# Kernel tuning notes

Measured on AMD Instinct MI355X. Metric: run time of the kernel, lower is better.

The kernel has to match this reference:

```python
import jax, jax.numpy as jnp
import numpy as np

LATENT_DIM = 512
NUM_EMBEDDINGS = 4096
COMMITMENT_COST = 0.25
N_TOKENS = 32768


def setup_inputs() -> dict:
    key = jax.random.key(0)
    k_z, k_e = jax.random.split(key)
    z = jax.random.normal(k_z, (N_TOKENS, LATENT_DIM), dtype=jnp.float32)
    # embedding.weight ~ U(-1/K, 1/K), matching the torch init
    emb = jax.random.uniform(
        k_e, (NUM_EMBEDDINGS, LATENT_DIM), dtype=jnp.float32,
        minval=-1.0 / NUM_EMBEDDINGS, maxval=1.0 / NUM_EMBEDDINGS)
    return {"z": z, "emb": emb}


def reference(z, emb):
    flat_z = z.reshape(-1, LATENT_DIM)  # [N, D]
    # squared L2 distances: ||z||^2 + ||e||^2 - 2 z.e^T  -> [N, K]
    distances = (
        jnp.sum(flat_z ** 2, axis=1, keepdims=True)
        + jnp.sum(emb ** 2, axis=1)
        - 2.0 * jnp.matmul(flat_z, emb.T)
    )
    encoding_indices = jnp.argmin(distances, axis=1)  # [N]
    quantized = emb[encoding_indices].reshape(z.shape)  # [N, D]

    q_latent_loss = jnp.mean((jax.lax.stop_gradient(quantized) - z) ** 2)
    commitment_loss = jnp.mean((quantized - jax.lax.stop_gradient(z)) ** 2)
    vq_loss = q_latent_loss + COMMITMENT_COST * commitment_loss

    # codebook usage perplexity (histogram instead of dense one-hot)
    n = flat_z.shape[0]
    counts = jnp.zeros((NUM_EMBEDDINGS,), jnp.float32).at[encoding_indices].add(1.0)
    avg_probs = counts / n
    perplexity = jnp.exp(-jnp.sum(avg_probs * jnp.log(avg_probs + 1e-10)))

    # straight-through estimator
    quantized_st = z + jax.lax.stop_gradient(quantized - z)
    return quantized_st, vq_loss, perplexity
```

## Files before the change

### kernel.cpp

```cpp
#include <hip/hip_runtime.h>

#define NTOK   32768
#define DIM    512
#define NCODE  4096
#define NELEM  (NTOK*DIM)
#define COMMIT 0.25
#define ESCALE 8192.0f
#define EINV   (1.0f/4096.0f)
#define KSCL   262144.0f
#define KOFF   65536.0f

#define OFF_Z8      0ULL
#define OFF_E8      16777216ULL
#define OFF_EN32    18874368ULL
#define OFF_ROWMIN  18890752ULL
#define OFF_COUNTS  19021824ULL
#define OFF_SSE     19038208ULL

typedef int   v8i  __attribute__((ext_vector_type(8)));
typedef float v16f __attribute__((ext_vector_type(16)));

#define GLOBAL_AS __attribute__((address_space(1)))
#define LDS_AS    __attribute__((address_space(3)))

__device__ __forceinline__ void gld16(const void* g, void* l) {
    __builtin_amdgcn_global_load_lds((const GLOBAL_AS unsigned int*)g,
                                     (LDS_AS unsigned int*)l, 16, 0, 0);
}

__global__ void conv_kernel(const float* __restrict__ z, const float* __restrict__ e,
                            unsigned* __restrict__ z8, unsigned* __restrict__ e8,
                            unsigned* __restrict__ counts, double* __restrict__ sse,
                            float* __restrict__ en32) {
    const int ZI = NELEM / 16;
    const int TI = ZI + (NCODE * DIM) / 16;
    int i = blockIdx.x * blockDim.x + threadIdx.x;
    if (i < NCODE) counts[i] = 0u;
    if (i < 256)   sse[i] = 0.0;
    if (i >= TI) return;
    const bool isEmb = (i >= ZI);
    const float4* src; unsigned* dst; int j; float sc;
    if (!isEmb) { src = (const float4*)z; dst = z8; j = i; sc = 1.0f; }
    else        { src = (const float4*)e; dst = e8; j = i - ZI; sc = ESCALE; }
    uint4 o;
    double nrm = 0.0;
#pragma unroll
    for (int q = 0; q < 4; q++) {
        float4 v = src[j * 4 + q];
        if (isEmb)
            nrm += (double)v.x*v.x + (double)v.y*v.y + (double)v.z*v.z + (double)v.w*v.w;
        int r = 0;
        r = __builtin_amdgcn_cvt_pk_fp8_f32(v.x * sc, v.y * sc, r, false);
        r = __builtin_amdgcn_cvt_pk_fp8_f32(v.z * sc, v.w * sc, r, true);
        (&o.x)[q] = (unsigned)r;
    }
    ((uint4*)dst)[j] = o;
    if (isEmb) {
#pragma unroll
        for (int off = 16; off; off >>= 1) nrm += __shfl_xor(nrm, off);
        if ((j & 31) == 0) en32[j >> 5] = (float)nrm;
    }
}

__global__ __launch_bounds__(256, 2)
void score_pass(const unsigned char* __restrict__ z8, const unsigned char* __restrict__ e8,
                const float* __restrict__ en32,
                const float* __restrict__ zf32, const float* __restrict__ embf,
                float* __restrict__ out, double* __restrict__ sse,
                unsigned* __restrict__ counts) {
    __shared__ __align__(16) unsigned char sB0[64 * 512];
    __shared__ __align__(16) unsigned char sB1[64 * 512];
    __shared__ __align__(16) float sEn[NCODE];
    const int tid = threadIdx.x;
    const int row0 = blockIdx.x * 64;
    const int wv = tid >> 6, ln = tid & 63;
    const int wm = wv & 1;
    const int wn = wv >> 1;
    const int c = ln & 31, h = ln >> 5;

#pragma unroll
    for (int s = 0; s < 8; s++) {
        int q = wv * 8 + s;
        int r = 2 * q + h;
        unsigned g = (unsigned)((ln & 31) ^ (r & 31));
        gld16(z8 + (size_t)(row0 + r) * 512 + g * 16u, sB1 + q * 1024);
    }
#pragma unroll
    for (int s = 0; s < 4; s++) {
        int chunk = wv * 4 + s;
        gld16((const unsigned char*)en32 + chunk * 1024 + (unsigned)(ln * 16),
              (unsigned char*)sEn + chunk * 1024);
    }

    unsigned eoff[8];
#pragma unroll
    for (int s = 0; s < 8; s++) {
        int q = wv * 8 + s;
        int r = 2 * q + h;
        unsigned g = (unsigned)((ln & 31) ^ (r & 31));
        eoff[s] = (unsigned)(r * 512) + g * 16u;
    }

    __builtin_amdgcn_sched_barrier(0);

#pragma unroll
    for (int s = 0; s < 8; s++)
        gld16(e8 + eoff[s], sB0 + (wv * 8 + s) * 1024);

    asm volatile("s_waitcnt vmcnt(8)" ::: "memory");
    __builtin_amdgcn_s_barrier();

    const int mrow = (wm * 32 + c) * 512;
    const int nrow = (wn * 32 + c) * 512;
    v8i za[8];
#pragma unroll
    for (int kt = 0; kt < 8; kt++) {
        int G = kt * 4 + 2 * h;
        uint4 x0 = *(const uint4*)(sB1 + mrow + (((G    ) ^ c) * 16));
        uint4 x1 = *(const uint4*)(sB1 + mrow + (((G + 1) ^ c) * 16));
        za[kt] = (v8i){(int)x0.x, (int)x0.y, (int)x0.z, (int)x0.w,
                       (int)x1.x, (int)x1.y, (int)x1.z, (int)x1.w};
    }
    asm volatile("s_waitcnt lgkmcnt(0)" ::: "memory");
    __builtin_amdgcn_s_barrier();

#pragma unroll
    for (int s = 0; s < 8; s++)
        gld16(e8 + 32768 + eoff[s], sB1 + (wv * 8 + s) * 1024);

    unsigned runmin[16];
#pragma unroll
    for (int reg = 0; reg < 16; reg++) runmin[reg] = 0xFFFFFFFFu;

    for (int ct = 0; ct < 64; ct++) {
        if (ct == 63) asm volatile("s_waitcnt vmcnt(0)" ::: "memory");
        else          asm volatile("s_waitcnt vmcnt(8)" ::: "memory");
        __builtin_amdgcn_s_barrier();

        const unsigned char* sB = (ct & 1) ? sB1 : sB0;
        float en = sEn[ct * 64 + wn * 32 + c];
        v16f acc0 = (v16f)(0.0f), acc1 = (v16f)(0.0f);
#pragma unroll
        for (int kt = 0; kt < 8; kt++) {
            int G = kt * 4 + 2 * h;
            uint4 y0 = *(const uint4*)(sB + nrow + (((G    ) ^ c) * 16));
            uint4 y1 = *(const uint4*)(sB + nrow + (((G + 1) ^ c) * 16));
            v8i b = (v8i){(int)y0.x, (int)y0.y, (int)y0.z, (int)y0.w,
                          (int)y1.x, (int)y1.y, (int)y1.z, (int)y1.w};
            if (kt & 1)
                acc1 = __builtin_amdgcn_mfma_scale_f32_32x32x64_f8f6f4(
                    za[kt], b, acc1, 0, 0, 0, 0x7F, 0, 0x7F);
            else
                acc0 = __builtin_amdgcn_mfma_scale_f32_32x32x64_f8f6f4(
                    za[kt], b, acc0, 0, 0, 0, 0x7F, 0, 0x7F);
        }

        unsigned n = (unsigned)(ct * 64 + wn * 32 + c);
#pragma unroll
        for (int reg = 0; reg < 16; reg++) {
            float s = en - (acc0[reg] + acc1[reg]) * EINV;
            unsigned kq = (unsigned)fmaf(s, KSCL, KOFF);
            unsigned p = (kq << 12) | n;
            runmin[reg] = runmin[reg] < p ? runmin[reg] : p;
        }

        asm volatile("s_waitcnt lgkmcnt(0)" ::: "memory");
        __builtin_amdgcn_s_barrier();

        if (ct < 62) {
            unsigned char* sD = (ct & 1) ? sB1 : sB0;
            const unsigned char* ebase = e8 + (size_t)(ct + 2) * 32768;
#pragma unroll
            for (int s = 0; s < 8; s++)
                gld16(ebase + eoff[s], sD + (wv * 8 + s) * 1024);
        }
    }

    __syncthreads();
    unsigned* tmp = (unsigned*)sB0;
#pragma unroll
    for (int reg = 0; reg < 16; reg++) {
        unsigned v = runmin[reg];
#pragma unroll
        for (int off = 1; off < 32; off <<= 1) {
            unsigned o = (unsigned)__shfl_xor((int)v, off);
            v = v < o ? v : o;
        }
        if (c == 0) {
            int rr = (reg & 3) + 8 * (reg >> 2) + 4 * h;
            tmp[(wm * 2 + wn) * 32 + rr] = v;
        }
    }
    __syncthreads();
    unsigned* rmin = (unsigned*)sB1;
    if (tid < 64) {
        int wmb = tid >> 5, rr = tid & 31;
        unsigned v0 = tmp[(wmb * 2 + 0) * 32 + rr];
        unsigned v1 = tmp[(wmb * 2 + 1) * 32 + rr];
        unsigned best = v0 < v1 ? v0 : v1;
        rmin[tid] = best & 0xFFFu;
        atomicAdd(&counts[best & 0xFFFu], 1u);
    }
    __syncthreads();

    const float4* zf = (const float4*)(zf32 + (size_t)row0 * 512);
    float4*       of = (float4*)(out + (size_t)row0 * 512);
    const float4* ef = (const float4*)embf;
    double loc = 0.0;
#pragma unroll 4
    for (int it = 0; it < 32; it++) {
        int idx = tid + it * 256;
        int row = idx >> 7, col = idx & 127;
        unsigned code = rmin[row];
        float4 zv = zf[idx];
        float4 q  = ef[code * 128 + col];
        float dx = q.x - zv.x, dy = q.y - zv.y, dz = q.z - zv.z, dw = q.w - zv.w;
        of[idx] = make_float4(zv.x + dx, zv.y + dy, zv.z + dz, zv.w + dw);
        loc += (double)dx*dx + (double)dy*dy + (double)dz*dz + (double)dw*dw;
    }
    for (int off = 32; off; off >>= 1) loc += __shfl_down(loc, off);
    double* sw = (double*)sEn;
    if (ln == 0) sw[wv] = loc;
    __syncthreads();
    if (tid == 0)
        atomicAdd(&sse[blockIdx.x & 255], sw[0] + sw[1] + sw[2] + sw[3]);
}

__global__ void finalize(const unsigned* __restrict__ counts, const double* __restrict__ sse,
                         float* __restrict__ out) {
    __shared__ double sh[256], sv[256];
    double h = 0.0;
    for (int b = threadIdx.x; b < NCODE; b += 256) {
        double p = (double)counts[b] / (double)NTOK;
        h += p * log(p + 1e-10);
    }
    sh[threadIdx.x] = h;
    sv[threadIdx.x] = sse[threadIdx.x];
    __syncthreads();
    for (int off = 128; off > 0; off >>= 1) {
        if (threadIdx.x < off) {
            sh[threadIdx.x] += sh[threadIdx.x + off];
            sv[threadIdx.x] += sv[threadIdx.x + off];
        }
        __syncthreads();
    }
    if (threadIdx.x == 0) {
        out[NELEM]     = (float)((1.0 + COMMIT) * sv[0] / (double)NELEM);
        out[NELEM + 1] = (float)exp(-sh[0]);
    }
}

extern "C" void kernel_launch(void* const* d_in, const int* in_sizes, int n_in,
                              void* d_out, int out_size, void* d_ws, size_t ws_size,
                              hipStream_t stream) {
    const float* z   = (const float*)d_in[0];
    const float* emb = (const float*)d_in[1];
    float* out = (float*)d_out;
    char* ws = (char*)d_ws;

    unsigned* z8 = (unsigned*)(ws + OFF_Z8);
    unsigned* e8 = (unsigned*)(ws + OFF_E8);
    float*    en32 = (float*)(ws + OFF_EN32);
    unsigned* counts = (unsigned*)(ws + OFF_COUNTS);
    double*   sse    = (double*)(ws + OFF_SSE);

    conv_kernel<<<(NELEM/16 + (NCODE*DIM)/16 + 255) / 256, 256, 0, stream>>>(
        z, emb, z8, e8, counts, sse, en32);

    score_pass<<<NTOK / 64, 256, 0, stream>>>((const unsigned char*)z8,
                                              (const unsigned char*)e8, en32,
                                              z, emb, out, sse, counts);

    finalize<<<1, 256, 0, stream>>>(counts, sse, out);
}
```

Measured before the change: 217.1 us.

## Fuse z FP8 conversion into score kernel, drop z8 workspace round-trip

The z-to-FP8 conversion now happens inside the score kernel. Each block loads its 64 fp32 rows, converts them in registers and writes them swizzled into LDS, so the prep kernel only converts the codebook. This removes a 16 MB fp8 write plus read-back through global memory and shrinks the first launch. In exchange, the block prologue now does synchronous fp32 loads, 4x the bytes of the previous async fp8 gld-to-LDS path, before the first barrier. That may expose latency that the earlier asynchronous load overlapped.

```diff
diff --git a/kernel.cpp b/kernel.cpp
--- a/kernel.cpp
+++ b/kernel.cpp
@@ -10,10 +10,8 @@
 #define KSCL   262144.0f
 #define KOFF   65536.0f
 
-#define OFF_Z8      0ULL
 #define OFF_E8      16777216ULL
 #define OFF_EN32    18874368ULL
-#define OFF_ROWMIN  18890752ULL
 #define OFF_COUNTS  19021824ULL
 #define OFF_SSE     19038208ULL
 
@@ -28,42 +26,33 @@
                                      (LDS_AS unsigned int*)l, 16, 0, 0);
 }
 
-__global__ void conv_kernel(const float* __restrict__ z, const float* __restrict__ e,
-                            unsigned* __restrict__ z8, unsigned* __restrict__ e8,
+__global__ void prep_kernel(const float* __restrict__ e,
+                            unsigned* __restrict__ e8,
                             unsigned* __restrict__ counts, double* __restrict__ sse,
                             float* __restrict__ en32) {
-    const int ZI = NELEM / 16;
-    const int TI = ZI + (NCODE * DIM) / 16;
     int i = blockIdx.x * blockDim.x + threadIdx.x;
     if (i < NCODE) counts[i] = 0u;
     if (i < 256)   sse[i] = 0.0;
-    if (i >= TI) return;
-    const bool isEmb = (i >= ZI);
-    const float4* src; unsigned* dst; int j; float sc;
-    if (!isEmb) { src = (const float4*)z; dst = z8; j = i; sc = 1.0f; }
-    else        { src = (const float4*)e; dst = e8; j = i - ZI; sc = ESCALE; }
+    const float4* src = (const float4*)e;
     uint4 o;
     double nrm = 0.0;
 #pragma unroll
     for (int q = 0; q < 4; q++) {
-        float4 v = src[j * 4 + q];
-        if (isEmb)
-            nrm += (double)v.x*v.x + (double)v.y*v.y + (double)v.z*v.z + (double)v.w*v.w;
+        float4 v = src[i * 4 + q];
+        nrm += (double)v.x*v.x + (double)v.y*v.y + (double)v.z*v.z + (double)v.w*v.w;
         int r = 0;
-        r = __builtin_amdgcn_cvt_pk_fp8_f32(v.x * sc, v.y * sc, r, false);
-        r = __builtin_amdgcn_cvt_pk_fp8_f32(v.z * sc, v.w * sc, r, true);
+        r = __builtin_amdgcn_cvt_pk_fp8_f32(v.x * ESCALE, v.y * ESCALE, r, false);
+        r = __builtin_amdgcn_cvt_pk_fp8_f32(v.z * ESCALE, v.w * ESCALE, r, true);
         (&o.x)[q] = (unsigned)r;
     }
-    ((uint4*)dst)[j] = o;
-    if (isEmb) {
-#pragma unroll
-        for (int off = 16; off; off >>= 1) nrm += __shfl_xor(nrm, off);
-        if ((j & 31) == 0) en32[j >> 5] = (float)nrm;
-    }
+    ((uint4*)e8)[i] = o;
+#pragma unroll
+    for (int off = 16; off; off >>= 1) nrm += __shfl_xor(nrm, off);
+    if ((i & 31) == 0) en32[i >> 5] = (float)nrm;
 }
 
 __global__ __launch_bounds__(256, 2)
-void score_pass(const unsigned char* __restrict__ z8, const unsigned char* __restrict__ e8,
+void score_pass(const unsigned char* __restrict__ e8,
                 const float* __restrict__ en32,
                 const float* __restrict__ zf32, const float* __restrict__ embf,
                 float* __restrict__ out, double* __restrict__ sse,
@@ -79,13 +68,6 @@
     const int c = ln & 31, h = ln >> 5;
 
 #pragma unroll
-    for (int s = 0; s < 8; s++) {
-        int q = wv * 8 + s;
-        int r = 2 * q + h;
-        unsigned g = (unsigned)((ln & 31) ^ (r & 31));
-        gld16(z8 + (size_t)(row0 + r) * 512 + g * 16u, sB1 + q * 1024);
-    }
-#pragma unroll
     for (int s = 0; s < 4; s++) {
         int chunk = wv * 4 + s;
         gld16((const unsigned char*)en32 + chunk * 1024 + (unsigned)(ln * 16),
@@ -100,15 +82,29 @@
         unsigned g = (unsigned)((ln & 31) ^ (r & 31));
         eoff[s] = (unsigned)(r * 512) + g * 16u;
     }
-
-    __builtin_amdgcn_sched_barrier(0);
-
 #pragma unroll
     for (int s = 0; s < 8; s++)
         gld16(e8 + eoff[s], sB0 + (wv * 8 + s) * 1024);
 
-    asm volatile("s_waitcnt vmcnt(8)" ::: "memory");
-    __builtin_amdgcn_s_barrier();
+    {
+        const float4* zsrc = (const float4*)(zf32 + (size_t)row0 * 512);
+#pragma unroll
+        for (int s = 0; s < 8; s++) {
+            int gi = tid + s * 256;
+            int r = gi >> 5, g = gi & 31;
+            uint4 o;
+#pragma unroll
+            for (int q = 0; q < 4; q++) {
+                float4 v = zsrc[4 * gi + q];
+                int rr = 0;
+                rr = __builtin_amdgcn_cvt_pk_fp8_f32(v.x, v.y, rr, false);
+                rr = __builtin_amdgcn_cvt_pk_fp8_f32(v.z, v.w, rr, true);
+                (&o.x)[q] = (unsigned)rr;
+            }
+            *(uint4*)(sB1 + r * 512 + ((g ^ (r & 31)) << 4)) = o;
+        }
+    }
+    __syncthreads();
 
     const int mrow = (wm * 32 + c) * 512;
     const int nrow = (wn * 32 + c) * 512;
@@ -258,17 +254,15 @@
     float* out = (float*)d_out;
     char* ws = (char*)d_ws;
 
-    unsigned* z8 = (unsigned*)(ws + OFF_Z8);
     unsigned* e8 = (unsigned*)(ws + OFF_E8);
     float*    en32 = (float*)(ws + OFF_EN32);
     unsigned* counts = (unsigned*)(ws + OFF_COUNTS);
     double*   sse    = (double*)(ws + OFF_SSE);
 
-    conv_kernel<<<(NELEM/16 + (NCODE*DIM)/16 + 255) / 256, 256, 0, stream>>>(
-        z, emb, z8, e8, counts, sse, en32);
-
-    score_pass<<<NTOK / 64, 256, 0, stream>>>((const unsigned char*)z8,
-                                              (const unsigned char*)e8, en32,
+    prep_kernel<<<(NCODE * DIM / 16) / 256, 256, 0, stream>>>(
+        emb, e8, counts, sse, en32);
+
+    score_pass<<<NTOK / 64, 256, 0, stream>>>((const unsigned char*)e8, en32,
                                               z, emb, out, sse, counts);
 
     finalize<<<1, 256, 0, stream>>>(counts, sse, out);
```

Result: faster. 212.7 us (-2.1%).
